# Optimization experiments

Hardware: AMD Instinct MI355X
Metric: run time of the kernel (lower is better)

The kernel has to match this reference:

```python
import jax, jax.numpy as jnp
import numpy as np

VOCAB = 45
MAX_LEN = 250
E = 1024
H = 8
F = 4096
L = 6
B = 32
S = 256


def layer_norm(x, g, b, eps=1e-5):
    m = x.mean(-1, keepdims=True)
    v = ((x - m) ** 2).mean(-1, keepdims=True)
    return (x - m) / jnp.sqrt(v + eps) * g + b


def setup_inputs() -> dict:
    key = jax.random.key(0)
    ks = jax.random.split(key, 20)
    s = 0.02
    inp = {
        "sequences": jax.random.randint(ks[0], (B, S), 1, VOCAB),  # avoid PAD id 0
        "token_emb": jax.random.normal(ks[1], (VOCAB, E), jnp.float32) * s,
        "dist_emb": jax.random.normal(ks[2], (MAX_LEN + 1, H), jnp.float32) * s,
        "Wqkv": jax.random.normal(ks[3], (L, 3 * E, E), jnp.float32) * s,
        "bqkv": jnp.zeros((L, 3 * E), jnp.float32),
        "Wo": jax.random.normal(ks[4], (L, E, E), jnp.float32) * s,
        "bo": jnp.zeros((L, E), jnp.float32),
        "W1": jax.random.normal(ks[5], (L, F, E), jnp.float32) * s,
        "b1": jnp.zeros((L, F), jnp.float32),
        "W2": jax.random.normal(ks[6], (L, E, F), jnp.float32) * s,
        "b2": jnp.zeros((L, E), jnp.float32),
        "ln1_g": jnp.ones((L, E), jnp.float32),
        "ln1_b": jnp.zeros((L, E), jnp.float32),
        "ln2_g": jnp.ones((L, E), jnp.float32),
        "ln2_b": jnp.zeros((L, E), jnp.float32),
        "fn_g": jnp.ones((E,), jnp.float32),
        "fn_b": jnp.zeros((E,), jnp.float32),
        "gen_W": jax.random.normal(ks[7], (VOCAB, E), jnp.float32) * s,
        "gen_b": jnp.zeros((VOCAB,), jnp.float32),
    }
    return inp


def reference(sequences, token_emb, dist_emb, Wqkv, bqkv, Wo, bo, W1, b1, W2, b2,
              ln1_g, ln1_b, ln2_g, ln2_b, fn_g, fn_b, gen_W, gen_b):
    Bsz, Slen = sequences.shape
    Emb = token_emb.shape[1]
    nH = dist_emb.shape[1]
    Dh = Emb // nH

    x = token_emb[sequences] * jnp.sqrt(jnp.float32(Emb))  # [B,S,E]

    idx = jnp.arange(Slen)
    dist = jnp.minimum(jnp.abs(idx[None, :] - idx[:, None]), dist_emb.shape[0] - 1)
    bias = jnp.transpose(dist_emb[dist], (2, 0, 1))  # [H,S,S]
    causal = idx[None, :] <= idx[:, None]  # key <= query (lower-triangular allowed)
    mask = jnp.where(causal[None, :, :], bias, jnp.float32(-1e9))  # [H,S,S]

    scale = 1.0 / jnp.sqrt(jnp.float32(Dh))
    nL = Wqkv.shape[0]
    for l in range(nL):
        qkv = x @ Wqkv[l].T + bqkv[l]  # [B,S,3E]
        q, k, v = jnp.split(qkv, 3, axis=-1)
        q = q.reshape(Bsz, Slen, nH, Dh)
        k = k.reshape(Bsz, Slen, nH, Dh)
        v = v.reshape(Bsz, Slen, nH, Dh)
        scores = jnp.einsum('bqhd,bkhd->bhqk', q, k) * scale + mask[None]
        attn = jax.nn.softmax(scores, axis=-1)
        o = jnp.einsum('bhqk,bkhd->bqhd', attn, v).reshape(Bsz, Slen, Emb)
        o = o @ Wo[l].T + bo[l]
        x = layer_norm(x + o, ln1_g[l], ln1_b[l])
        h = jax.nn.gelu(x @ W1[l].T + b1[l], approximate=False)
        h = h @ W2[l].T + b2[l]
        x = layer_norm(x + h, ln2_g[l], ln2_b[l])

    x = layer_norm(x, fn_g, fn_b)
    logits = x @ gen_W.T + gen_b  # [B,S,VOCAB]
    return logits
```

## Files before the change

kernel.cpp:

```cpp
#include <hip/hip_runtime.h>
#include <hip/hip_bf16.h>

typedef __hip_bfloat16 bf16;
typedef __attribute__((ext_vector_type(8))) short short8;
typedef __attribute__((ext_vector_type(4))) float f32x4;

#define GLB_AS(p) ((const __attribute__((address_space(1))) void*)(p))
#define LDS_AS(p) ((__attribute__((address_space(3))) void*)(p))

template<int EPI>
__global__ __launch_bounds__(256) void gemm_bf16(
    const bf16* __restrict__ Ain, const bf16* __restrict__ Bin, void* __restrict__ Cv,
    int K, int lda, int ldb, int ldc,
    long sAo, long sAi, long sBo, long sBi, long sCo, long sCi, int nInner,
    const float* __restrict__ bias, const float* __restrict__ demb,
    float scale)
{
    __shared__ __align__(16) bf16 Als[128 * 64];
    __shared__ __align__(16) bf16 Bls[128 * 64];

    const int z  = blockIdx.z;
    const int zo = z / nInner;
    const int zi = z - zo * nInner;
    const bf16* A = Ain + zo * sAo + zi * sAi;
    const bf16* B = Bin + zo * sBo + zi * sBi;
    const long coff = zo * sCo + zi * sCi;

    int m_t, n_t;
    if (EPI == 3) {
        m_t = (blockIdx.x + 1) >> 1;
        n_t = blockIdx.x >> 1;
    } else {
        const int Mt = gridDim.x, Nt = gridDim.y;
        if (Mt >= 8) {
            const int pid = blockIdx.y * Mt + blockIdx.x;
            const int grpsz = 8 * Nt;
            const int grp = pid / grpsz;
            const int first = grp * 8;
            int rem = Mt - first; if (rem > 8) rem = 8;
            const int loc = pid - grp * grpsz;
            m_t = first + loc % rem;
            n_t = loc / rem;
        } else { m_t = blockIdx.x; n_t = blockIdx.y; }
    }
    const int m0 = m_t * 128;
    const int n0 = n_t * 128;

    const int Keff = (EPI == 4) ? (m_t + 1) * 128 : K;

    const int tid  = threadIdx.x;
    const int wave = tid >> 6;
    const int lane = tid & 63;
    const int wm = (wave >> 1) * 64;
    const int wn = (wave & 1) * 64;

    f32x4 acc[4][4];
#pragma unroll
    for (int i = 0; i < 4; ++i)
#pragma unroll
        for (int j = 0; j < 4; ++j) acc[i][j] = (f32x4){0.f, 0.f, 0.f, 0.f};

    const int srow = lane >> 3;
    const int scol = (((lane & 7) ^ srow) << 3);

    for (int k0 = 0; k0 < Keff; k0 += 64) {
        __syncthreads();
#pragma unroll
        for (int c = 0; c < 4; ++c) {
            const int chunk = (wave << 2) + c;
            const int row = (chunk << 3) + srow;
            const bf16* ga = A + (long)(m0 + row) * lda + k0 + scol;
            const bf16* gb = B + (long)(n0 + row) * ldb + k0 + scol;
            __builtin_amdgcn_global_load_lds(GLB_AS(ga), LDS_AS(&Als[chunk << 9]), 16, 0, 0);
            __builtin_amdgcn_global_load_lds(GLB_AS(gb), LDS_AS(&Bls[chunk << 9]), 16, 0, 0);
        }
        __syncthreads();

#pragma unroll
        for (int kk = 0; kk < 2; ++kk) {
            const int CB = (kk << 2) + (lane >> 4);
            const int r = lane & 15;
            short8 afr[4], bfr[4];
#pragma unroll
            for (int i = 0; i < 4; ++i) {
                const int ar = wm + (i << 4) + r;
                afr[i] = *(const short8*)&Als[ar * 64 + ((CB ^ (ar & 7)) << 3)];
            }
#pragma unroll
            for (int j = 0; j < 4; ++j) {
                const int br = wn + (j << 4) + r;
                bfr[j] = *(const short8*)&Bls[br * 64 + ((CB ^ (br & 7)) << 3)];
            }
#pragma unroll
            for (int i = 0; i < 4; ++i)
#pragma unroll
                for (int j = 0; j < 4; ++j)
                    acc[i][j] = __builtin_amdgcn_mfma_f32_16x16x32_bf16(
                        afr[i], bfr[j], acc[i][j], 0, 0, 0);
        }
    }

    const int ccol = lane & 15;
    const int crow = (lane >> 4) << 2;
#pragma unroll
    for (int i = 0; i < 4; ++i) {
#pragma unroll
        for (int j = 0; j < 4; ++j) {
            const int col  = n0 + wn + (j << 4) + ccol;
            const int rowb = m0 + wm + (i << 4) + crow;
#pragma unroll
            for (int r2 = 0; r2 < 4; ++r2) {
                const int row = rowb + r2;
                float v = acc[i][j][r2];
                const long cidx = coff + (long)row * ldc + col;
                if (EPI == 3) {
                    int d0 = row - col;
                    int ad = d0 < 0 ? -d0 : d0;
                    if (ad > 250) ad = 250;
                    ((bf16*)Cv)[cidx] = __float2bfloat16(v * scale + demb[ad * 8 + zi]);
                } else if (EPI == 0) {
                    if (bias) v += bias[col];
                    ((float*)Cv)[cidx] = v;
                } else if (EPI == 1 || EPI == 4) {
                    if (bias) v += bias[col];
                    ((bf16*)Cv)[cidx] = __float2bfloat16(v);
                } else {
                    v += bias[col];
                    v = 0.5f * v * (1.0f + erff(v * 0.70710678118f));
                    ((bf16*)Cv)[cidx] = __float2bfloat16(v);
                }
            }
        }
    }
}

__global__ void cast4_kernel(const float* __restrict__ s0, const float* __restrict__ s1,
                             const float* __restrict__ s2, const float* __restrict__ s3,
                             bf16* __restrict__ d0, bf16* __restrict__ d1,
                             bf16* __restrict__ d2, bf16* __restrict__ d3,
                             long n0, long n1, long n2, long n3)
{
    long i = (long)blockIdx.x * blockDim.x + threadIdx.x;
    const float* s; bf16* d; long base;
    if (i < n0)                { s = s0; d = d0; base = 0; }
    else if (i < n0 + n1)      { s = s1; d = d1; base = n0; }
    else if (i < n0 + n1 + n2) { s = s2; d = d2; base = n0 + n1; }
    else if (i < n0+n1+n2+n3)  { s = s3; d = d3; base = n0 + n1 + n2; }
    else return;
    const long j = i - base;
    f32x4 v = *(const f32x4*)(s + j * 4);
    bf16 t[4] = {__float2bfloat16(v[0]), __float2bfloat16(v[1]),
                 __float2bfloat16(v[2]), __float2bfloat16(v[3])};
    *(short4*)(d + j * 4) = *(const short4*)t;
}

__global__ void embed_kernel(const int* __restrict__ seq, const float* __restrict__ emb,
                             float* __restrict__ x, bf16* __restrict__ xb)
{
    const long t = blockIdx.x;
    const int tok = seq[t];
    const int tid = threadIdx.x;
    f32x4 v = *(const f32x4*)(emb + (long)tok * 1024 + tid * 4);
    v *= 32.0f;
    *(f32x4*)(x + t * 1024 + tid * 4) = v;
    bf16 tq[4] = {__float2bfloat16(v[0]), __float2bfloat16(v[1]),
                  __float2bfloat16(v[2]), __float2bfloat16(v[3])};
    *(short4*)(xb + t * 1024 + tid * 4) = *(const short4*)tq;
}

__global__ void softmax_kernel(const bf16* __restrict__ scores, bf16* __restrict__ probs)
{
    const long row = (long)blockIdx.x * 4 + (threadIdx.x >> 6);
    const int q = (int)(row & 255);
    const int lane = threadIdx.x & 63;
    const int kbase = lane * 4;
    short4 sv = *(const short4*)(scores + row * 256 + kbase);
    const bf16* sp = (const bf16*)&sv;
    float v0 = (kbase + 0 <= q) ? __bfloat162float(sp[0]) : -1e30f;
    float v1 = (kbase + 1 <= q) ? __bfloat162float(sp[1]) : -1e30f;
    float v2 = (kbase + 2 <= q) ? __bfloat162float(sp[2]) : -1e30f;
    float v3 = (kbase + 3 <= q) ? __bfloat162float(sp[3]) : -1e30f;
    float m = fmaxf(fmaxf(v0, v1), fmaxf(v2, v3));
#pragma unroll
    for (int off = 32; off; off >>= 1) m = fmaxf(m, __shfl_xor(m, off));
    float e0 = (kbase + 0 <= q) ? __expf(v0 - m) : 0.f;
    float e1 = (kbase + 1 <= q) ? __expf(v1 - m) : 0.f;
    float e2 = (kbase + 2 <= q) ? __expf(v2 - m) : 0.f;
    float e3 = (kbase + 3 <= q) ? __expf(v3 - m) : 0.f;
    float s = e0 + e1 + e2 + e3;
#pragma unroll
    for (int off = 32; off; off >>= 1) s += __shfl_xor(s, off);
    const float inv = 1.0f / s;
    bf16 tq[4] = {__float2bfloat16(e0 * inv), __float2bfloat16(e1 * inv),
                  __float2bfloat16(e2 * inv), __float2bfloat16(e3 * inv)};
    *(short4*)(probs + row * 256 + kbase) = *(const short4*)tq;
}

__global__ void transpose_v(const bf16* __restrict__ qkv, bf16* __restrict__ vt)
{
    __shared__ bf16 tile[32][33];
    const int bh = blockIdx.y;
    const int st = blockIdx.x & 7;
    const int dt = blockIdx.x >> 3;
    const int tx = threadIdx.x & 31;
    const int ty = threadIdx.x >> 5;
    const int b = bh >> 3, h = bh & 7;
    const bf16* src = qkv + ((long)b * 256) * 3072 + 2048 + h * 128 + dt * 32;
#pragma unroll
    for (int i = 0; i < 4; ++i) {
        const int s = st * 32 + ty * 4 + i;
        tile[ty * 4 + i][tx] = src[(long)s * 3072 + tx];
    }
    __syncthreads();
    bf16* dst = vt + ((long)bh * 128 + dt * 32) * 256 + st * 32;
#pragma unroll
    for (int i = 0; i < 4; ++i) {
        const int dl = ty * 4 + i;
        dst[(long)dl * 256 + tx] = tile[tx][dl];
    }
}

__global__ void ln_kernel(const float* __restrict__ x, const bf16* __restrict__ res,
                          const float* __restrict__ g, const float* __restrict__ bta,
                          float* __restrict__ outf, bf16* __restrict__ outb,
                          int has_res, int has_bf)
{
    const long t = blockIdx.x;
    const int tid = threadIdx.x;
    f32x4 v = *(const f32x4*)(x + t * 1024 + tid * 4);
    if (has_res) {
        short4 rv = *(const short4*)(res + t * 1024 + tid * 4);
        const bf16* rp = (const bf16*)&rv;
#pragma unroll
        for (int q = 0; q < 4; ++q) v[q] += __bfloat162float(rp[q]);
    }
    float s  = v[0] + v[1] + v[2] + v[3];
    float ss = v[0]*v[0] + v[1]*v[1] + v[2]*v[2] + v[3]*v[3];
#pragma unroll
    for (int off = 32; off; off >>= 1) {
        s  += __shfl_xor(s, off);
        ss += __shfl_xor(ss, off);
    }
    __shared__ float red[8];
    const int w = tid >> 6;
    if ((tid & 63) == 0) { red[w] = s; red[4 + w] = ss; }
    __syncthreads();
    s  = red[0] + red[1] + red[2] + red[3];
    ss = red[4] + red[5] + red[6] + red[7];
    const float mean = s * (1.0f / 1024.0f);
    const float var  = ss * (1.0f / 1024.0f) - mean * mean;
    const float rstd = rsqrtf(var + 1e-5f);
    f32x4 gv = *(const f32x4*)(g + tid * 4);
    f32x4 bv = *(const f32x4*)(bta + tid * 4);
    f32x4 o;
#pragma unroll
    for (int q = 0; q < 4; ++q) o[q] = (v[q] - mean) * rstd * gv[q] + bv[q];
    *(f32x4*)(outf + t * 1024 + tid * 4) = o;
    if (has_bf) {
        bf16 tq[4] = {__float2bfloat16(o[0]), __float2bfloat16(o[1]),
                      __float2bfloat16(o[2]), __float2bfloat16(o[3])};
        *(short4*)(outb + t * 1024 + tid * 4) = *(const short4*)tq;
    }
}

__global__ void gen_kernel(const float* __restrict__ xf, const float* __restrict__ W,
                           const float* __restrict__ bias, float* __restrict__ out)
{
    const long t = (long)blockIdx.x * 4 + (threadIdx.x >> 6);
    const int lane = threadIdx.x & 63;
    const float* xr = xf + t * 1024;
    float xv[16];
#pragma unroll
    for (int j = 0; j < 16; ++j) xv[j] = xr[lane + 64 * j];
    for (int n = 0; n < 45; ++n) {
        const float* wr = W + (long)n * 1024;
        float a = 0.f;
#pragma unroll
        for (int j = 0; j < 16; ++j) a += xv[j] * wr[lane + 64 * j];
#pragma unroll
        for (int off = 32; off; off >>= 1) a += __shfl_xor(a, off);
        if (lane == 0) out[t * 45 + n] = a + bias[n];
    }
}

extern "C" void kernel_launch(void* const* d_in, const int* in_sizes, int n_in,
                              void* d_out, int out_size, void* d_ws, size_t ws_size,
                              hipStream_t stream)
{
    (void)in_sizes; (void)n_in; (void)out_size; (void)ws_size;
    const int*   seq  = (const int*)d_in[0];
    const float* temb = (const float*)d_in[1];
    const float* demb = (const float*)d_in[2];
    const float* Wqkv = (const float*)d_in[3];
    const float* bqkv = (const float*)d_in[4];
    const float* Wo   = (const float*)d_in[5];
    const float* bo   = (const float*)d_in[6];
    const float* W1   = (const float*)d_in[7];
    const float* b1   = (const float*)d_in[8];
    const float* W2   = (const float*)d_in[9];
    const float* b2   = (const float*)d_in[10];
    const float* ln1g = (const float*)d_in[11];
    const float* ln1b = (const float*)d_in[12];
    const float* ln2g = (const float*)d_in[13];
    const float* ln2b = (const float*)d_in[14];
    const float* fng  = (const float*)d_in[15];
    const float* fnb  = (const float*)d_in[16];
    const float* genW = (const float*)d_in[17];
    const float* genb = (const float*)d_in[18];
    float* out = (float*)d_out;

    char* ws = (char*)d_ws;
    size_t off = 0;
    auto alloc = [&](size_t bytes) -> char* {
        char* p = ws + off;
        off += (bytes + 255) & ~(size_t)255;
        return p;
    };

    bf16*  wqkv_l = (bf16*)alloc(3072ULL * 1024 * 2);
    bf16*  wo_l   = (bf16*)alloc(1024ULL * 1024 * 2);
    bf16*  w1_l   = (bf16*)alloc(4096ULL * 1024 * 2);
    bf16*  w2_l   = (bf16*)alloc(1024ULL * 4096 * 2);
    float* x      = (float*)alloc(8192ULL * 1024 * 4);
    bf16*  xb     = (bf16*)alloc(8192ULL * 1024 * 2);
    char*  qkvreg = alloc(8192ULL * 3072 * 2);
    char*  R      = alloc(8192ULL * 4096 * 2);
    bf16*  tmpb   = (bf16*)alloc(8192ULL * 1024 * 2);

    bf16*  qkvb   = (bf16*)qkvreg;
    bf16*  attnb  = (bf16*)qkvreg;
    float* lnout  = (float*)qkvreg;
    bf16*  scoreb = (bf16*)R;
    bf16*  probs  = (bf16*)(R + 8192ULL * 4096);
    bf16*  vt     = (bf16*)R;
    bf16*  hbuf   = (bf16*)R;

    const dim3 blk(256);

    embed_kernel<<<8192, blk, 0, stream>>>(seq, temb, x, xb);

    for (int l = 0; l < 6; ++l) {
        cast4_kernel<<<12288, blk, 0, stream>>>(
            Wqkv + (long)l * 3072 * 1024, Wo + (long)l * 1024 * 1024,
            W1 + (long)l * 4096 * 1024,   W2 + (long)l * 4096 * 1024,
            wqkv_l, wo_l, w1_l, w2_l,
            786432, 262144, 1048576, 1048576);

        gemm_bf16<1><<<dim3(64, 24, 1), blk, 0, stream>>>(xb, wqkv_l, qkvb,
            1024, 1024, 1024, 3072, 0, 0, 0, 0, 0, 0, 1,
            bqkv + (long)l * 3072, nullptr, 0.f);

        gemm_bf16<3><<<dim3(3, 1, 256), blk, 0, stream>>>(qkvb, qkvb + 1024, scoreb,
            128, 3072, 3072, 256,
            786432, 128, 786432, 128, 524288, 65536, 8,
            nullptr, demb, 0.08838834764831845f);

        softmax_kernel<<<16384, blk, 0, stream>>>(scoreb, probs);
        transpose_v<<<dim3(32, 256), blk, 0, stream>>>(qkvb, vt);

        gemm_bf16<4><<<dim3(2, 1, 256), blk, 0, stream>>>(probs, vt, attnb,
            256, 256, 256, 1024,
            524288, 65536, 262144, 32768, 262144, 128, 8,
            nullptr, nullptr, 0.f);

        gemm_bf16<1><<<dim3(64, 8, 1), blk, 0, stream>>>(attnb, wo_l, tmpb,
            1024, 1024, 1024, 1024, 0, 0, 0, 0, 0, 0, 1,
            bo + (long)l * 1024, nullptr, 0.f);

        ln_kernel<<<8192, blk, 0, stream>>>(x, tmpb, ln1g + (long)l * 1024,
                                            ln1b + (long)l * 1024, x, xb, 1, 1);

        gemm_bf16<2><<<dim3(64, 32, 1), blk, 0, stream>>>(xb, w1_l, hbuf,
            1024, 1024, 1024, 4096, 0, 0, 0, 0, 0, 0, 1,
            b1 + (long)l * 4096, nullptr, 0.f);

        gemm_bf16<1><<<dim3(64, 8, 1), blk, 0, stream>>>(hbuf, w2_l, tmpb,
            4096, 4096, 4096, 1024, 0, 0, 0, 0, 0, 0, 1,
            b2 + (long)l * 1024, nullptr, 0.f);

        ln_kernel<<<8192, blk, 0, stream>>>(x, tmpb, ln2g + (long)l * 1024,
                                            ln2b + (long)l * 1024, x, xb, 1, 1);
    }

    ln_kernel<<<8192, blk, 0, stream>>>(x, nullptr, fng, fnb, lnout, nullptr, 0, 0);
    gen_kernel<<<2048, blk, 0, stream>>>(lnout, genW, genb, out);
}
```

Measured before the change: 2.863 ms.

## Add 256x256 eight-wave pipelined bf16 GEMM for projection and FFN layers

Adds a new GEMM kernel that uses 256x256 output tiles and 512 threads (8 waves), with double-buffered LDS filled by direct global-to-LDS loads that are staged two k-steps ahead. It also uses XOR-swizzled LDS layout, an XCD-aware block remapping with grouped tile ordering, and s_setprio around the MFMA bursts. The four dense layer GEMMs (QKV, output projection, FFN1, FFN2) now use it in place of the 128-tile kernel. The aim is more data reuse per tile and better overlap of loads with MFMA work. In exchange it needs large LDS and register use, and it assumes M and N divide evenly into 256-wide tiles.

```diff
diff --git a/kernel.cpp b/kernel.cpp
--- a/kernel.cpp
+++ b/kernel.cpp
@@ -7,6 +7,145 @@
 
 #define GLB_AS(p) ((const __attribute__((address_space(1))) void*)(p))
 #define LDS_AS(p) ((__attribute__((address_space(3))) void*)(p))
+
+template<int EPI>
+__global__ __launch_bounds__(512, 2) void gemm8p(
+    const bf16* __restrict__ A, const bf16* __restrict__ Bm, bf16* __restrict__ C,
+    int K, int lda, int ldb, int ldc, const float* __restrict__ bias)
+{
+    __shared__ __align__(16) bf16 Als[2][2][8192];
+    __shared__ __align__(16) bf16 Bls[2][2][8192];
+
+    const int tid  = threadIdx.x;
+    const int wave = tid >> 6;
+    const int lane = tid & 63;
+    const int wr = wave >> 2;
+    const int wc = wave & 3;
+
+    const int Mt = gridDim.x, Nt = gridDim.y;
+    int pid = blockIdx.y * Mt + blockIdx.x;
+    const int cpx = (Mt * Nt) >> 3;
+    pid = (pid & 7) * cpx + (pid >> 3);
+    int m_t, n_t;
+    {
+        const int grpsz = 8 * Nt;
+        const int grp = pid / grpsz;
+        const int first = grp * 8;
+        int rem = Mt - first; if (rem > 8) rem = 8;
+        const int loc = pid - grp * grpsz;
+        m_t = first + loc % rem;
+        n_t = loc / rem;
+    }
+    const int m0 = m_t << 8;
+    const int n0 = n_t << 8;
+    const int nt = K >> 6;
+
+    const int s_r  = tid >> 2;
+    const int s_sl = ((tid & 3) ^ ((tid >> 3) & 3)) << 3;
+    const bf16* As0 = A  + (long)(m0 + s_r) * lda + s_sl;
+    const bf16* Bs0 = Bm + (long)(n0 + s_r) * ldb + s_sl;
+    const long ldal = (long)lda << 7;
+    const long ldbl = (long)ldb << 7;
+    char* AB = (char*)Als;
+    char* BB = (char*)Bls;
+    const int wofs = wave << 10;
+
+#define STAGE_A(d, kh, tt) do { \
+    const bf16* g_ = As0 + ((long)(tt) << 6) + ((kh) << 5); \
+    char* dst_ = AB + ((((d) << 1) + (kh)) << 14) + wofs; \
+    __builtin_amdgcn_global_load_lds(GLB_AS(g_), LDS_AS(dst_), 16, 0, 0); \
+    __builtin_amdgcn_global_load_lds(GLB_AS(g_ + ldal), LDS_AS(dst_ + 8192), 16, 0, 0); \
+  } while (0)
+#define STAGE_B(d, kh, tt) do { \
+    const bf16* g_ = Bs0 + ((long)(tt) << 6) + ((kh) << 5); \
+    char* dst_ = BB + ((((d) << 1) + (kh)) << 14) + wofs; \
+    __builtin_amdgcn_global_load_lds(GLB_AS(g_), LDS_AS(dst_), 16, 0, 0); \
+    __builtin_amdgcn_global_load_lds(GLB_AS(g_ + ldbl), LDS_AS(dst_ + 8192), 16, 0, 0); \
+  } while (0)
+#define BAR() do { asm volatile("" ::: "memory"); \
+    __builtin_amdgcn_s_barrier(); asm volatile("" ::: "memory"); } while (0)
+
+    STAGE_B(0, 0, 0); STAGE_A(0, 0, 0); STAGE_B(0, 1, 0); STAGE_A(0, 1, 0);
+    STAGE_B(1, 0, 1); STAGE_A(1, 0, 1); STAGE_B(1, 1, 1);
+
+    f32x4 acc[8][4];
+#pragma unroll
+    for (int i = 0; i < 8; ++i)
+#pragma unroll
+        for (int j = 0; j < 4; ++j) acc[i][j] = (f32x4){0.f, 0.f, 0.f, 0.f};
+
+    const int fr  = lane & 15;
+    const int swz = (((lane >> 4) ^ ((lane >> 1) & 3)) << 4);
+    const int aoff = (wr << 13) + fr * 64 + swz;
+    const int boff = (wc << 12) + fr * 64 + swz;
+
+    asm volatile("s_waitcnt vmcnt(6)" ::: "memory");
+    __builtin_amdgcn_s_barrier();
+    asm volatile("" ::: "memory");
+
+    int d = 0;
+    for (int t = 0; t < nt; ++t, d ^= 1) {
+        short8 b[4];
+#pragma unroll
+        for (int p = 0; p < 4; ++p) {
+            const int kh = p >> 1, rh = p & 1;
+            const char* Ahb = AB + (((d << 1) + kh) << 14);
+            const char* Bhb = BB + (((d << 1) + kh) << 14);
+            short8 a[4];
+#pragma unroll
+            for (int i = 0; i < 4; ++i)
+                a[i] = *(const short8*)(Ahb + aoff + rh * 4096 + i * 1024);
+            if ((p & 1) == 0) {
+#pragma unroll
+                for (int j = 0; j < 4; ++j)
+                    b[j] = *(const short8*)(Bhb + boff + j * 1024);
+            }
+            if (p == 0)      { if (t + 1 < nt) STAGE_A(d ^ 1, 1, t + 1); }
+            else if (p == 1) { if (t + 2 < nt) STAGE_B(d, 0, t + 2); }
+            else if (p == 2) { if (t + 2 < nt) STAGE_A(d, 0, t + 2); }
+            else             { if (t + 2 < nt) STAGE_B(d, 1, t + 2); }
+            BAR();
+            asm volatile("s_waitcnt lgkmcnt(0)" ::: "memory");
+            __builtin_amdgcn_sched_barrier(0);
+            __builtin_amdgcn_s_setprio(1);
+#pragma unroll
+            for (int i = 0; i < 4; ++i)
+#pragma unroll
+                for (int j = 0; j < 4; ++j)
+                    acc[rh * 4 + i][j] = __builtin_amdgcn_mfma_f32_16x16x32_bf16(
+                        a[i], b[j], acc[rh * 4 + i][j], 0, 0, 0);
+            __builtin_amdgcn_s_setprio(0);
+            if (p == 3 && t < nt - 1) {
+                if (t == nt - 2) asm volatile("s_waitcnt vmcnt(0)" ::: "memory");
+                else             asm volatile("s_waitcnt vmcnt(6)" ::: "memory");
+            }
+            BAR();
+        }
+    }
+#undef STAGE_A
+#undef STAGE_B
+#undef BAR
+
+    const int ccol = lane & 15;
+    const int crow = (lane >> 4) << 2;
+    const int colb  = n0 + (wc << 6) + ccol;
+    const int rowbb = m0 + (wr << 7) + crow;
+#pragma unroll
+    for (int j = 0; j < 4; ++j) {
+        const int col = colb + (j << 4);
+        const float bv = bias[col];
+#pragma unroll
+        for (int i = 0; i < 8; ++i) {
+            const int rowb = rowbb + (i << 4);
+#pragma unroll
+            for (int r2 = 0; r2 < 4; ++r2) {
+                float v = acc[i][j][r2] + bv;
+                if (EPI == 2) v = 0.5f * v * (1.0f + erff(v * 0.70710678118f));
+                C[(long)(rowb + r2) * ldc + col] = __float2bfloat16(v);
+            }
+        }
+    }
+}
 
 template<int EPI>
 __global__ __launch_bounds__(256) void gemm_bf16(
@@ -336,6 +475,7 @@
     bf16*  hbuf   = (bf16*)R;
 
     const dim3 blk(256);
+    const dim3 blk8(512);
 
     embed_kernel<<<8192, blk, 0, stream>>>(seq, temb, x, xb);
 
@@ -346,9 +486,8 @@
             wqkv_l, wo_l, w1_l, w2_l,
             786432, 262144, 1048576, 1048576);
 
-        gemm_bf16<1><<<dim3(64, 24, 1), blk, 0, stream>>>(xb, wqkv_l, qkvb,
-            1024, 1024, 1024, 3072, 0, 0, 0, 0, 0, 0, 1,
-            bqkv + (long)l * 3072, nullptr, 0.f);
+        gemm8p<1><<<dim3(32, 12), blk8, 0, stream>>>(xb, wqkv_l, qkvb,
+            1024, 1024, 1024, 3072, bqkv + (long)l * 3072);
 
         gemm_bf16<3><<<dim3(3, 1, 256), blk, 0, stream>>>(qkvb, qkvb + 1024, scoreb,
             128, 3072, 3072, 256,
@@ -363,20 +502,17 @@
             524288, 65536, 262144, 32768, 262144, 128, 8,
             nullptr, nullptr, 0.f);
 
-        gemm_bf16<1><<<dim3(64, 8, 1), blk, 0, stream>>>(attnb, wo_l, tmpb,
-            1024, 1024, 1024, 1024, 0, 0, 0, 0, 0, 0, 1,
-            bo + (long)l * 1024, nullptr, 0.f);
+        gemm8p<1><<<dim3(32, 4), blk8, 0, stream>>>(attnb, wo_l, tmpb,
+            1024, 1024, 1024, 1024, bo + (long)l * 1024);
 
         ln_kernel<<<8192, blk, 0, stream>>>(x, tmpb, ln1g + (long)l * 1024,
                                             ln1b + (long)l * 1024, x, xb, 1, 1);
 
-        gemm_bf16<2><<<dim3(64, 32, 1), blk, 0, stream>>>(xb, w1_l, hbuf,
-            1024, 1024, 1024, 4096, 0, 0, 0, 0, 0, 0, 1,
-            b1 + (long)l * 4096, nullptr, 0.f);
-
-        gemm_bf16<1><<<dim3(64, 8, 1), blk, 0, stream>>>(hbuf, w2_l, tmpb,
-            4096, 4096, 4096, 1024, 0, 0, 0, 0, 0, 0, 1,
-            b2 + (long)l * 1024, nullptr, 0.f);
+        gemm8p<2><<<dim3(32, 16), blk8, 0, stream>>>(xb, w1_l, hbuf,
+            1024, 1024, 1024, 4096, b1 + (long)l * 4096);
+
+        gemm8p<1><<<dim3(32, 4), blk8, 0, stream>>>(hbuf, w2_l, tmpb,
+            4096, 4096, 4096, 1024, b2 + (long)l * 1024);
 
         ln_kernel<<<8192, blk, 0, stream>>>(x, tmpb, ln2g + (long)l * 1024,
                                             ln2b + (long)l * 1024, x, xb, 1, 1);
```

New measurement: 3.016 ms. 1.05x slower.
